# Performance work log

Measured on AMD Instinct MI355X. Metric: run time of the kernel, lower is better.

Reference implementation:

```python
import jax, jax.numpy as jnp
import numpy as np

EMBED = 1024
HEADS = 16
HIDDEN = 4 * EMBED
EPS = 1e-5


def layer_norm(x, g, b):
    mu = jnp.mean(x, axis=-1, keepdims=True)
    var = jnp.var(x, axis=-1, keepdims=True)
    return (x - mu) * jax.lax.rsqrt(var + EPS) * g + b


def setup_inputs() -> dict:
    key = jax.random.key(0)
    ks = jax.random.split(key, 8)
    s = EMBED ** -0.5
    return {
        "x": jax.random.normal(ks[0], (4, 2048, EMBED), dtype=jnp.float32),
        "ln1_g": jnp.ones((EMBED,), jnp.float32),
        "ln1_b": jnp.zeros((EMBED,), jnp.float32),
        "qkv_w": jax.random.normal(ks[1], (3 * EMBED, EMBED), jnp.float32) * s,
        "out_w": jax.random.normal(ks[2], (EMBED, EMBED), jnp.float32) * s,
        "out_b": jnp.zeros((EMBED,), jnp.float32),
        "ln2_g": jnp.ones((EMBED,), jnp.float32),
        "ln2_b": jnp.zeros((EMBED,), jnp.float32),
        "fc1_w": jax.random.normal(ks[3], (HIDDEN, EMBED), jnp.float32) * s,
        "fc1_b": jnp.zeros((HIDDEN,), jnp.float32),
        "fc2_w": jax.random.normal(ks[4], (EMBED, HIDDEN), jnp.float32) * (HIDDEN ** -0.5),
        "fc2_b": jnp.zeros((EMBED,), jnp.float32),
    }


def reference(x, ln1_g, ln1_b, qkv_w, out_w, out_b, ln2_g, ln2_b, fc1_w, fc1_b, fc2_w, fc2_b):
    B, N, C = x.shape
    hd = C // HEADS
    # --- attention (pre-LN); note: NO 1/sqrt(d) scaling, matching the source ---
    h = layer_norm(x, ln1_g, ln1_b)
    qkv = h @ qkv_w.T                                  # [B,N,3C]
    qkv = qkv.reshape(B, N, 3, HEADS, hd).transpose(2, 0, 3, 1, 4)
    q, k, v = qkv[0], qkv[1], qkv[2]                   # [B,H,N,hd]
    attn = jax.nn.softmax(jnp.einsum("bhqd,bhkd->bhqk", q, k), axis=-1)
    o = jnp.einsum("bhqk,bhkd->bhqd", attn, v)
    o = o.transpose(0, 2, 1, 3).reshape(B, N, C)
    x = x + o @ out_w.T + out_b
    # --- MLP (exact erf GELU, matching nn.GELU default) ---
    h = layer_norm(x, ln2_g, ln2_b)
    h = jax.nn.gelu(h @ fc1_w.T + fc1_b, approximate=False)
    x = x + h @ fc2_w.T + fc2_b
    return x
```

## Files before the change

### kernel.cpp

```cpp
#include <hip/hip_runtime.h>
#include <cstdint>


using short8 = __attribute__((ext_vector_type(8))) short;
using f32x4  = __attribute__((ext_vector_type(4))) float;
using f32x16 = __attribute__((ext_vector_type(16))) float;

#define EMBED  1024
#define HIDDEN 4096
#define SEQ    2048
#define NTOK   8192

__device__ __forceinline__ ushort f2bf(float x) {
  union { float f; uint32_t u; } v; v.f = x;
  uint32_t r = v.u + 0x7fffu + ((v.u >> 16) & 1u);
  return (ushort)(r >> 16);
}

__device__ __forceinline__ uint32_t pkbf(float lo, float hi) {
  uint32_t r;
  asm("v_cvt_pk_bf16_f32 %0, %1, %2" : "=v"(r) : "v"(lo), "v"(hi));
  return r;
}

__device__ __forceinline__ void gload16(const void* g, void* l) {
  __builtin_amdgcn_global_load_lds((__attribute__((address_space(1))) void*)(g),
                                   (__attribute__((address_space(3))) void*)(l), 16, 0, 0);
}

template<int N> __device__ __forceinline__ void vwait() {
  asm volatile("s_waitcnt vmcnt(%0)" :: "n"(N) : "memory");
}
__device__ __forceinline__ void lgkm0() {
  asm volatile("s_waitcnt lgkmcnt(0)" ::: "memory");
}
__device__ __forceinline__ void fence_bar() {
  asm volatile("" ::: "memory");
  __builtin_amdgcn_s_barrier();
  asm volatile("" ::: "memory");
}

__device__ __forceinline__ f32x4 mfma16(short8 a, short8 b, f32x4 c) {
  return __builtin_amdgcn_mfma_f32_16x16x32_bf16(a, b, c, 0, 0, 0);
}
__device__ __forceinline__ f32x16 mfma32(short8 a, short8 b, f32x16 c) {
  return __builtin_amdgcn_mfma_f32_32x32x16_bf16(a, b, c, 0, 0, 0);
}
__device__ __forceinline__ f32x16 zero16() {
  f32x16 z = {0.f,0.f,0.f,0.f,0.f,0.f,0.f,0.f,0.f,0.f,0.f,0.f,0.f,0.f,0.f,0.f};
  return z;
}

__global__ __launch_bounds__(256) void cvt_bf16_kernel(const float* __restrict__ in,
                                                       ushort* __restrict__ out, int n4) {
  int i = blockIdx.x * 256 + threadIdx.x;
  if (i < n4) {
    float4 v = reinterpret_cast<const float4*>(in)[i];
    ushort4 o; o.x = f2bf(v.x); o.y = f2bf(v.y); o.z = f2bf(v.z); o.w = f2bf(v.w);
    reinterpret_cast<ushort4*>(out)[i] = o;
  }
}

__global__ __launch_bounds__(256) void ln_kernel(const float* __restrict__ x,
                                                 const float* __restrict__ g,
                                                 const float* __restrict__ b,
                                                 ushort* __restrict__ out) {
  const int row = blockIdx.x, tid = threadIdx.x;
  const float4 xv = reinterpret_cast<const float4*>(x + (size_t)row * EMBED)[tid];
  float s  = xv.x + xv.y + xv.z + xv.w;
  float s2 = xv.x*xv.x + xv.y*xv.y + xv.z*xv.z + xv.w*xv.w;
  #pragma unroll
  for (int off = 32; off >= 1; off >>= 1) { s += __shfl_xor(s, off); s2 += __shfl_xor(s2, off); }
  __shared__ float ps[4], ps2[4];
  if ((tid & 63) == 0) { ps[tid >> 6] = s; ps2[tid >> 6] = s2; }
  __syncthreads();
  s  = ps[0] + ps[1] + ps[2] + ps[3];
  s2 = ps2[0] + ps2[1] + ps2[2] + ps2[3];
  const float mu  = s * (1.f / EMBED);
  const float var = s2 * (1.f / EMBED) - mu * mu;
  const float rs  = rsqrtf(var + 1e-5f);
  const float4 gv = reinterpret_cast<const float4*>(g)[tid];
  const float4 bv = reinterpret_cast<const float4*>(b)[tid];
  ushort4 o;
  o.x = f2bf((xv.x - mu) * rs * gv.x + bv.x);
  o.y = f2bf((xv.y - mu) * rs * gv.y + bv.y);
  o.z = f2bf((xv.z - mu) * rs * gv.z + bv.z);
  o.w = f2bf((xv.w - mu) * rs * gv.w + bv.w);
  reinterpret_cast<ushort4*>(out + (size_t)row * EMBED)[tid] = o;
}

template<int EPI, bool SQ>
__global__ __launch_bounds__(512) void gemm256(const ushort* __restrict__ A,
                                               const ushort* __restrict__ B,
                                               const float* __restrict__ bias,
                                               const float* __restrict__ res,
                                               ushort* __restrict__ outb,
                                               float* __restrict__ outf,
                                               int M, int N, int K, int gx) {
  constexpr int BN   = SQ ? 256 : 128;
  constexpr int MP   = SQ ? 8 : 4;
  constexpr int NPH  = SQ ? 2 : 1;
  constexpr int LPT  = SQ ? 4 : 3;
  constexpr int NB   = LPT - 2;
  constexpr int ABUF = 256 * 32;
  constexpr int BBUF = BN * 32;
  __shared__ ushort lds[4][ABUF + BBUF];

  const int nwg = gridDim.x;
  const int b0  = blockIdx.x;
  const int p = b0 & 7, li = b0 >> 3;
  int mt, nt;
  if ((gx & 7) == 0) {
    const int g = gx >> 3;
    mt = p * g + (li % g);
    nt = li / g;
  } else {
    const int g = (nwg / gx) >> 3;
    nt = p * g + (li % g);
    mt = li / g;
  }
  const int m0 = mt * 256;
  const int n0 = nt * BN;

  const int tid = threadIdx.x, lane = tid & 63, wave = tid >> 6;
  const int wm = (SQ ? (wave >> 2) : (wave >> 1)) * (MP * 16);
  const int wn = (SQ ? (wave & 3) : (wave & 1)) * 64;
  const int l15 = lane & 15, l4 = lane >> 4;
  const int NT = K >> 5;

  const ushort* aSrc[2];
  const ushort* bSrc[NB];
  #pragma unroll
  for (int rd = 0; rd < 2; ++rd) {
    const int slot = rd * 512 + tid;
    const int r = slot >> 2;
    const int cs = (slot & 3) ^ ((r >> 1) & 3);
    aSrc[rd] = A + (size_t)(m0 + r) * K + cs * 8;
  }
  #pragma unroll
  for (int rd = 0; rd < NB; ++rd) {
    const int slot = rd * 512 + tid;
    const int r = slot >> 2;
    const int cs = (slot & 3) ^ ((r >> 1) & 3);
    bSrc[rd] = B + (size_t)(n0 + r) * K + cs * 8;
  }
  auto stageA = [&](int buf, int rd) { gload16(aSrc[rd], &lds[buf][(rd * 512 + tid) * 8]); };
  auto stageB = [&](int buf, int rd) { gload16(bSrc[rd], &lds[buf][ABUF + (rd * 512 + tid) * 8]); };
  auto advance = [&]() {
    #pragma unroll
    for (int rd = 0; rd < 2; ++rd) aSrc[rd] += 32;
    #pragma unroll
    for (int rd = 0; rd < NB; ++rd) bSrc[rd] += 32;
  };

  #pragma unroll
  for (int t = 0; t < 3; ++t) {
    stageA(t, 0); stageA(t, 1);
    #pragma unroll
    for (int rd = 0; rd < NB; ++rd) stageB(t, rd);
    advance();
  }
  vwait<2 * LPT>();
  fence_bar();

  f32x4 acc[MP][4] = {};

  auto doTile = [&](int q, bool st, int wsel) {
    const ushort* bA = &lds[q][0];
    const ushort* bB = &lds[q][ABUF];
    const int sbuf = (q + 3) & 3;
    short8 bf[4];
    #pragma unroll
    for (int j = 0; j < 4; ++j) {
      const int rb = wn + j * 16 + l15;
      bf[j] = *reinterpret_cast<const short8*>(&bB[rb * 32 + ((l4 ^ ((rb >> 1) & 3)) * 8)]);
    }
    #pragma unroll
    for (int ph = 0; ph < NPH; ++ph) {
      short8 af[4];
      #pragma unroll
      for (int i = 0; i < 4; ++i) {
        const int ra = wm + (ph * 4 + i) * 16 + l15;
        af[i] = *reinterpret_cast<const short8*>(&bA[ra * 32 + ((l4 ^ ((ra >> 1) & 3)) * 8)]);
      }
      if (st) {
        if constexpr (SQ) {
          if (ph == 0) { stageA(sbuf, 0); stageA(sbuf, 1); }
          else         { stageB(sbuf, 0); stageB(sbuf, 1); }
        } else {
          stageA(sbuf, 0); stageA(sbuf, 1); stageB(sbuf, 0);
        }
      }
      fence_bar();
      __builtin_amdgcn_s_setprio(1);
      #pragma unroll
      for (int i = 0; i < 4; ++i)
        #pragma unroll
        for (int j = 0; j < 4; ++j)
          acc[ph * 4 + i][j] = mfma16(af[i], bf[j], acc[ph * 4 + i][j]);
      __builtin_amdgcn_s_setprio(0);
      if (ph == NPH - 1) {
        if (st) advance();
        if (wsel == 0)      vwait<2 * LPT>();
        else if (wsel == 1) vwait<LPT>();
        else if (wsel == 2) vwait<0>();
      }
      fence_bar();
    }
  };

  for (int u0 = 0; u0 < NT - 4; u0 += 4) {
    doTile(0, true, 0); doTile(1, true, 0); doTile(2, true, 0); doTile(3, true, 0);
  }
  doTile(0, true, 0); doTile(1, false, 1); doTile(2, false, 2); doTile(3, false, 3);

  #pragma unroll
  for (int i = 0; i < MP; ++i)
    #pragma unroll
    for (int j = 0; j < 4; ++j)
      #pragma unroll
      for (int r = 0; r < 4; ++r) {
        const int row = m0 + wm + i * 16 + l4 * 4 + r;
        const int col = n0 + wn + j * 16 + l15;
        const size_t idx = (size_t)row * N + col;
        float v = acc[i][j][r];
        if constexpr (EPI == 0) {
          outb[idx] = f2bf(v);
        } else if constexpr (EPI == 1) {
          outf[idx] = v + bias[col] + res[idx];
        } else {
          v += bias[col];
          v = 0.5f * v * (1.f + erff(v * 0.70710678118654752f));
          outb[idx] = f2bf(v);
        }
      }
}

#define KVB 64
#define NTT (SEQ / KVB)

__global__ __launch_bounds__(512, 4) void attn_kernel(const ushort* __restrict__ qk,
                                                      const ushort* __restrict__ vt,
                                                      ushort* __restrict__ outp) {
  const int tid = threadIdx.x, lane = tid & 63, wq = tid >> 6;
  const int hi = lane >> 5, lo = lane & 31;
  const int b = blockIdx.x >> 4, h = blockIdx.x & 15;
  const int q0 = blockIdx.y * 256;

  __shared__ ushort sK[2][64 * 64];
  __shared__ ushort sVt[2][64 * 64];
  __shared__ float sBc[8][32];

  short8 qf[4];
  #pragma unroll
  for (int kc = 0; kc < 4; ++kc)
    qf[kc] = *reinterpret_cast<const short8*>(
        qk + (size_t)(b * SEQ + q0 + wq * 32 + lo) * 2048 + h * 64 + kc * 16 + hi * 8);

  auto STAGE = [&](int bb, int kt) {
    const int r = tid >> 3;
    const int c = (tid & 7) ^ (r & 7);
    gload16(qk + (size_t)(b * SEQ + kt + r) * 2048 + 1024 + h * 64 + c * 8,
            &sK[bb][wq * 64 * 8]);
    gload16(vt + (size_t)(h * 64 + r) * 8192 + b * SEQ + kt + c * 8,
            &sVt[bb][wq * 64 * 8]);
  };

  f32x16 acc[2];
  acc[0] = zero16(); acc[1] = zero16();
  float mst = -1e30f, lst = 0.f;

  STAGE(0, 0);
  for (int t = 0; t < NTT; ++t) {
    const int cur = t & 1;
    __syncthreads();
    if (t + 1 < NTT) STAGE(cur ^ 1, (t + 1) * KVB);

    short8 kf[2][4];
    #pragma unroll
    for (int kvb = 0; kvb < 2; ++kvb)
      #pragma unroll
      for (int kc = 0; kc < 4; ++kc) {
        const int row = kvb * 32 + lo, ch = kc * 2 + hi;
        kf[kvb][kc] = *reinterpret_cast<const short8*>(
            &sK[cur][(row * 8 + (ch ^ (row & 7))) * 8]);
      }

    f32x16 st[2];
    #pragma unroll
    for (int kvb = 0; kvb < 2; ++kvb) {
      f32x16 tq = zero16();
      tq = mfma32(kf[kvb][0], qf[0], tq);
      tq = mfma32(kf[kvb][1], qf[1], tq);
      tq = mfma32(kf[kvb][2], qf[2], tq);
      tq = mfma32(kf[kvb][3], qf[3], tq);
      st[kvb] = tq;
    }
    float pm = fmaxf(st[0][0], st[0][1]);
    #pragma unroll
    for (int r = 2; r < 16; ++r) pm = fmaxf(pm, st[0][r]);
    #pragma unroll
    for (int r = 0; r < 16; ++r) pm = fmaxf(pm, st[1][r]);
    pm = fmaxf(pm, __shfl_xor(pm, 32));
    if (__any(pm > mst + 8.f)) {
      const float mn = fmaxf(mst, pm);
      const float al = __expf(mst - mn);
      mst = mn; lst *= al;
      sBc[wq][lo] = al;
      lgkm0();
      #pragma unroll
      for (int g = 0; g < 4; ++g) {
        const f32x4 a4 = *reinterpret_cast<const f32x4*>(&sBc[wq][g * 8 + hi * 4]);
        #pragma unroll
        for (int j = 0; j < 4; ++j) {
          acc[0][g * 4 + j] *= a4[j];
          acc[1][g * 4 + j] *= a4[j];
        }
      }
    }
    #pragma unroll
    for (int kvb = 0; kvb < 2; ++kvb)
      #pragma unroll
      for (int r = 0; r < 16; ++r)
        st[kvb][r] = __expf(st[kvb][r] - mst);
    {
      const f32x16 sv = st[0] + st[1];
      float sum = ((sv[0] + sv[1]) + (sv[2] + sv[3])) + ((sv[4] + sv[5]) + (sv[6] + sv[7]))
                + ((sv[8] + sv[9]) + (sv[10] + sv[11])) + ((sv[12] + sv[13]) + (sv[14] + sv[15]));
      sum += __shfl_xor(sum, 32);
      lst += sum;
    }
    short8 pa[4];
    #pragma unroll
    for (int kvb = 0; kvb < 2; ++kvb)
      #pragma unroll
      for (int f = 0; f < 2; ++f) {
        uint32_t wa = pkbf(st[kvb][f * 8 + 0], st[kvb][f * 8 + 1]);
        uint32_t wb = pkbf(st[kvb][f * 8 + 2], st[kvb][f * 8 + 3]);
        uint32_t wc = pkbf(st[kvb][f * 8 + 4], st[kvb][f * 8 + 5]);
        uint32_t wd = pkbf(st[kvb][f * 8 + 6], st[kvb][f * 8 + 7]);
        asm volatile("v_permlane32_swap_b32 %0, %1" : "+v"(wa), "+v"(wc));
        asm volatile("v_permlane32_swap_b32 %0, %1" : "+v"(wb), "+v"(wd));
        union { uint32_t w[4]; short8 v; } u;
        u.w[0] = wa; u.w[1] = wb; u.w[2] = wc; u.w[3] = wd;
        pa[kvb * 2 + f] = u.v;
      }

    #pragma unroll
    for (int db = 0; db < 2; ++db) {
      short8 vb[4];
      #pragma unroll
      for (int k4 = 0; k4 < 4; ++k4) {
        const int row = db * 32 + lo, ch = k4 * 2 + hi;
        vb[k4] = *reinterpret_cast<const short8*>(
            &sVt[cur][(row * 8 + (ch ^ (row & 7))) * 8]);
      }
      acc[db] = mfma32(pa[0], vb[0], acc[db]);
      acc[db] = mfma32(pa[1], vb[1], acc[db]);
      acc[db] = mfma32(pa[2], vb[2], acc[db]);
      acc[db] = mfma32(pa[3], vb[3], acc[db]);
    }
  }

  sBc[wq][lo] = 1.f / lst;
  lgkm0();
  #pragma unroll
  for (int g = 0; g < 4; ++g) {
    const f32x4 r4 = *reinterpret_cast<const f32x4*>(&sBc[wq][g * 8 + hi * 4]);
    #pragma unroll
    for (int j = 0; j < 4; ++j) {
      const int qrow = q0 + wq * 32 + g * 8 + hi * 4 + j;
      #pragma unroll
      for (int db = 0; db < 2; ++db)
        outp[(size_t)(b * SEQ + qrow) * EMBED + h * 64 + db * 32 + lo] =
            f2bf(acc[db][g * 4 + j] * r4[j]);
    }
  }
}

extern "C" void kernel_launch(void* const* d_in, const int* in_sizes, int n_in,
                              void* d_out, int out_size, void* d_ws, size_t ws_size,
                              hipStream_t stream) {
  const float* x     = (const float*)d_in[0];
  const float* ln1_g = (const float*)d_in[1];
  const float* ln1_b = (const float*)d_in[2];
  const float* qkv_w = (const float*)d_in[3];
  const float* out_w = (const float*)d_in[4];
  const float* out_b = (const float*)d_in[5];
  const float* ln2_g = (const float*)d_in[6];
  const float* ln2_b = (const float*)d_in[7];
  const float* fc1_w = (const float*)d_in[8];
  const float* fc1_b = (const float*)d_in[9];
  const float* fc2_w = (const float*)d_in[10];
  const float* fc2_b = (const float*)d_in[11];
  float* out = (float*)d_out;
  char* ws = (char*)d_ws;

  ushort* qkvw = (ushort*)(ws);
  ushort* outw = (ushort*)(ws + 6291456);
  ushort* fc1w = (ushort*)(ws + 8388608);
  ushort* fc2w = (ushort*)(ws + 16777216);
  float*  x1   = (float*) (ws + 25165824);
  ushort* hbuf = (ushort*)(ws + 58720256);
  ushort* qkbuf= (ushort*)(ws + 75497472);
  ushort* vtbuf= (ushort*)(ws + 109051904);
  ushort* obuf = (ushort*)(ws + 125829120);
  ushort* gbuf = qkbuf;

  cvt_bf16_kernel<<<3072, 256, 0, stream>>>(qkv_w, qkvw, 3 * EMBED * EMBED / 4);
  cvt_bf16_kernel<<<1024, 256, 0, stream>>>(out_w, outw, EMBED * EMBED / 4);
  cvt_bf16_kernel<<<4096, 256, 0, stream>>>(fc1_w, fc1w, HIDDEN * EMBED / 4);
  cvt_bf16_kernel<<<4096, 256, 0, stream>>>(fc2_w, fc2w, EMBED * HIDDEN / 4);

  ln_kernel<<<NTOK, 256, 0, stream>>>(x, ln1_g, ln1_b, hbuf);
  gemm256<0, true><<<256, 512, 0, stream>>>(hbuf, qkvw, nullptr, nullptr,
                                            qkbuf, nullptr, NTOK, 2 * EMBED, EMBED, 32);
  gemm256<0, false><<<256, 512, 0, stream>>>(qkvw + 2048 * 1024, hbuf, nullptr, nullptr,
                                             vtbuf, nullptr, EMBED, NTOK, EMBED, 4);
  attn_kernel<<<dim3(64, 8), 512, 0, stream>>>(qkbuf, vtbuf, obuf);
  gemm256<1, false><<<256, 512, 0, stream>>>(obuf, outw, out_b, x,
                                             nullptr, x1, NTOK, EMBED, EMBED, 32);
  ln_kernel<<<NTOK, 256, 0, stream>>>(x1, ln2_g, ln2_b, hbuf);
  gemm256<2, true><<<512, 512, 0, stream>>>(hbuf, fc1w, fc1_b, nullptr,
                                            gbuf, nullptr, NTOK, HIDDEN, EMBED, 32);
  gemm256<1, false><<<256, 512, 0, stream>>>(gbuf, fc2w, fc2_b, x1,
                                             nullptr, out, NTOK, EMBED, HIDDEN, 32);
}
```

Baseline: 384.5 us.

## Add 128x128-tile GEMM kernel and use it for the MLP fc1 and fc2 layers

Adds a smaller 128x128-tile, 256-thread bf16 MFMA GEMM with double-buffered LDS, swizzled loads and XCD-aware tile mapping. The two MLP GEMMs now use it instead of the 256x256 kernel. The fc2 launch goes from 256 to 512 workgroups and fc1 from 512 to 2048. The aim is better occupancy and load balance across CUs, at the cost of less operand reuse per tile and more global traffic.

```diff
diff --git a/kernel.cpp b/kernel.cpp
--- a/kernel.cpp
+++ b/kernel.cpp
@@ -236,6 +236,117 @@
       }
 }
 
+template<int EPI>
+__global__ __launch_bounds__(256) void gemm128(const ushort* __restrict__ A,
+                                               const ushort* __restrict__ B,
+                                               const float* __restrict__ bias,
+                                               const float* __restrict__ res,
+                                               ushort* __restrict__ outb,
+                                               float* __restrict__ outf,
+                                               int M, int N, int K, int gx) {
+  __shared__ ushort sA[2][128 * 32];
+  __shared__ ushort sB[2][128 * 32];
+
+  const int nwg = gridDim.x;
+  const int b0  = blockIdx.x;
+  const int p = b0 & 7, li = b0 >> 3;
+  int mt, nt;
+  if ((gx & 7) == 0) {
+    const int g = gx >> 3;
+    mt = p * g + (li % g);
+    nt = li / g;
+  } else {
+    const int g = (nwg / gx) >> 3;
+    nt = p * g + (li % g);
+    mt = li / g;
+  }
+  const int m0 = mt * 128;
+  const int n0 = nt * 128;
+
+  const int tid = threadIdx.x, lane = tid & 63, wave = tid >> 6;
+  const int wm = (wave >> 1) * 64, wn = (wave & 1) * 64;
+  const int l15 = lane & 15, l4 = lane >> 4;
+  const int NT = K >> 5;
+
+  const ushort* aS[2];
+  const ushort* bS[2];
+  #pragma unroll
+  for (int rd = 0; rd < 2; ++rd) {
+    const int slot = rd * 256 + tid, r = slot >> 2;
+    const int cs = (slot & 3) ^ ((r >> 1) & 3);
+    aS[rd] = A + (size_t)(m0 + r) * K + cs * 8;
+    bS[rd] = B + (size_t)(n0 + r) * K + cs * 8;
+  }
+  int aOff[4], bOff[4];
+  #pragma unroll
+  for (int i = 0; i < 4; ++i) {
+    const int ra = wm + i * 16 + l15;
+    aOff[i] = ra * 32 + ((l4 ^ ((ra >> 1) & 3)) * 8);
+    const int rb = wn + i * 16 + l15;
+    bOff[i] = rb * 32 + ((l4 ^ ((rb >> 1) & 3)) * 8);
+  }
+
+  auto STAGE = [&](int buf) {
+    #pragma unroll
+    for (int rd = 0; rd < 2; ++rd) {
+      gload16(aS[rd], &sA[buf][(rd * 256 + tid) * 8]);
+      gload16(bS[rd], &sB[buf][(rd * 256 + tid) * 8]);
+    }
+    aS[0] += 32; aS[1] += 32; bS[0] += 32; bS[1] += 32;
+  };
+
+  f32x4 acc[4][4] = {};
+
+  auto COMP = [&](int buf) {
+    short8 af[4], bf[4];
+    #pragma unroll
+    for (int i = 0; i < 4; ++i) {
+      af[i] = *reinterpret_cast<const short8*>(&sA[buf][aOff[i]]);
+      bf[i] = *reinterpret_cast<const short8*>(&sB[buf][bOff[i]]);
+    }
+    __builtin_amdgcn_s_setprio(1);
+    #pragma unroll
+    for (int i = 0; i < 4; ++i)
+      #pragma unroll
+      for (int j = 0; j < 4; ++j)
+        acc[i][j] = mfma16(af[i], bf[j], acc[i][j]);
+    __builtin_amdgcn_s_setprio(0);
+  };
+
+  STAGE(0);
+  for (int u = 0; u < NT; u += 2) {
+    vwait<0>();
+    fence_bar();
+    if (u + 1 < NT) STAGE(1);
+    COMP(0);
+    vwait<0>();
+    fence_bar();
+    if (u + 2 < NT) STAGE(0);
+    COMP(1);
+  }
+
+  #pragma unroll
+  for (int i = 0; i < 4; ++i)
+    #pragma unroll
+    for (int j = 0; j < 4; ++j)
+      #pragma unroll
+      for (int r = 0; r < 4; ++r) {
+        const int row = m0 + wm + i * 16 + l4 * 4 + r;
+        const int col = n0 + wn + j * 16 + l15;
+        const size_t idx = (size_t)row * N + col;
+        float v = acc[i][j][r];
+        if constexpr (EPI == 0) {
+          outb[idx] = f2bf(v);
+        } else if constexpr (EPI == 1) {
+          outf[idx] = v + bias[col] + res[idx];
+        } else {
+          v += bias[col];
+          v = 0.5f * v * (1.f + erff(v * 0.70710678118654752f));
+          outb[idx] = f2bf(v);
+        }
+      }
+}
+
 #define KVB 64
 #define NTT (SEQ / KVB)
 
@@ -421,8 +532,8 @@
   gemm256<1, false><<<256, 512, 0, stream>>>(obuf, outw, out_b, x,
                                              nullptr, x1, NTOK, EMBED, EMBED, 32);
   ln_kernel<<<NTOK, 256, 0, stream>>>(x1, ln2_g, ln2_b, hbuf);
-  gemm256<2, true><<<512, 512, 0, stream>>>(hbuf, fc1w, fc1_b, nullptr,
-                                            gbuf, nullptr, NTOK, HIDDEN, EMBED, 32);
-  gemm256<1, false><<<256, 512, 0, stream>>>(gbuf, fc2w, fc2_b, x1,
-                                             nullptr, out, NTOK, EMBED, HIDDEN, 32);
-}
+  gemm128<2><<<2048, 256, 0, stream>>>(hbuf, fc1w, fc1_b, nullptr,
+                                       gbuf, nullptr, NTOK, HIDDEN, EMBED, 64);
+  gemm128<1><<<512, 256, 0, stream>>>(gbuf, fc2w, fc2_b, x1,
+                                      nullptr, out, NTOK, EMBED, HIDDEN, 64);
+}
```

Result: slower. 408.1 us (+6.1%).
